# Kernel tuning notes

Measured on AMD Instinct MI355X. Metric: run time of the kernel, lower is better.

## Reference

```python
import jax, jax.numpy as jnp
import numpy as np

TEMPERATURE = 0.07
TIME_THRESH = 5.0 * 1e6  # microseconds


def setup_inputs() -> dict:
    key = jax.random.key(0)
    k1, k2, k3 = jax.random.split(key, 3)
    B, D = 8192, 512
    desc = jax.random.normal(k1, (B, D), dtype=jnp.float32)
    desc = desc / jnp.linalg.norm(desc, axis=-1, keepdims=True)  # module expects normalized descriptors
    seq_ids = jax.random.randint(k2, (B,), 0, 64, dtype=jnp.int64)
    time_mid = jax.random.randint(k3, (B,), 0, 20_000_000, dtype=jnp.int64)
    return {"descriptors": desc, "seq_ids": seq_ids, "time_mid": time_mid}


def reference(descriptors, seq_ids, time_mid):
    B = descriptors.shape[0]
    # [B, B] temperature-scaled cosine similarities
    logits = jnp.matmul(descriptors, descriptors.T) / TEMPERATURE

    eye = jnp.eye(B, dtype=bool)
    same_seq = seq_ids[:, None] == seq_ids[None, :]
    close_time = jnp.abs(time_mid[:, None] - time_mid[None, :]).astype(jnp.float32) < TIME_THRESH
    pos_mask = same_seq & close_time & ~eye  # positives
    offdiag = ~eye                            # positives + negatives = denominator support

    # denominator per row i: log sum_{j != i} exp(logits[i, j])
    denom_lse = jax.nn.logsumexp(jnp.where(offdiag, logits, -jnp.inf), axis=1)  # [B]

    # per positive pair (i, j): -log( exp(l_ij) / denom_i ) = denom_lse_i - l_ij
    pair_loss = jnp.where(pos_mask, denom_lse[:, None] - logits, 0.0)
    num_pos = jnp.sum(pos_mask)
    loss = jnp.sum(pair_loss) / jnp.maximum(num_pos, 1).astype(pair_loss.dtype)
    return loss
```

## Files before the change

kernel.cpp:

```cpp
#include <hip/hip_runtime.h>
#include <math.h>

#define TILE 128

typedef __attribute__((ext_vector_type(4))) float f32x4;
typedef __attribute__((ext_vector_type(2))) long long llong2;

#define INV_T    14.285714285714286f
#define K2C      20.60992915f
#define K2C8     0.32203014296875f
#define INV_T64  0.22321428571428573f
#define TIME_THR 5000000

__device__ __forceinline__ unsigned pack_bf16x2(float lo, float hi) {
  unsigned a = __float_as_uint(lo);
  unsigned b = __float_as_uint(hi);
  a = (a + 0x7FFFu + ((a >> 16) & 1u)) >> 16;
  b = (b + 0x7FFFu + ((b >> 16) & 1u)) & 0xFFFF0000u;
  return b | a;
}

__device__ __forceinline__ unsigned f32_to_e4m3(float x) {
  unsigned u = __float_as_uint(x);
  unsigned s = (u >> 24) & 0x80u;
  int e = (int)((u >> 23) & 0xffu) - 127;
  unsigned m = u & 0x7fffffu;
  if (e < -9) return s;
  if (e < -6) {
    int sh = 20 + (-6 - e);
    unsigned full = (1u << 23) | m;
    unsigned q = full >> sh;
    unsigned rem = full & ((1u << sh) - 1u);
    unsigned half = 1u << (sh - 1);
    if (rem > half || (rem == half && (q & 1u))) q++;
    return s | q;
  }
  unsigned q = m >> 20;
  unsigned rem = m & 0xfffffu;
  if (rem > 0x80000u || (rem == 0x80000u && (q & 1u))) q++;
  int ee = e;
  if (q == 8u) { q = 0u; ee++; }
  if (ee > 8 || (ee == 8 && q == 7u)) return s | 0x7eu;
  return s | (unsigned)((ee + 7) << 3) | q;
}

__device__ __forceinline__ void gl_lds16(const void* g, void* l) {
  __builtin_amdgcn_global_load_lds(
      (const __attribute__((address_space(1))) unsigned int*)g,
      (__attribute__((address_space(3))) unsigned int*)l, 16, 0, 0);
}

template <int MODE>
__device__ __forceinline__ void infonce_body(
    const float* __restrict__ desc, const unsigned char* __restrict__ desc8,
    const int* __restrict__ seq, const int* __restrict__ tmid,
    float* __restrict__ p_se, float* __restrict__ p_ps,
    float* __restrict__ p_pc, int B, int D, int NB) {
  __shared__ __align__(16) unsigned char lA8[2][TILE][64];
  __shared__ __align__(16) unsigned char lB8[2][TILE][64];
  __shared__ int mseq_r[TILE], mtim_r[TILE], mseq_c[TILE], mtim_c[TILE];

  const int T = NB * (NB + 1) / 2;
  int t = blockIdx.x;
  if ((T & 7) == 0) t = (t & 7) * (T >> 3) + (t >> 3);
  float fn = (float)NB + 0.5f;
  int r = (int)(fn - sqrtf(fmaxf(fn * fn - 2.0f * (float)t, 0.0f)));
  if (r < 0) r = 0;
  if (r > NB - 1) r = NB - 1;
  auto Sf = [NB](int rr) { return rr * NB - ((rr * (rr - 1)) >> 1); };
  while (r > 0 && Sf(r) > t) --r;
  while (r < NB - 1 && Sf(r + 1) <= t) ++r;
  const int rb = r;
  const int cb = rb + (t - Sf(rb));
  const bool upper = (cb != rb);

  const int row0 = rb * TILE;
  const int col0 = cb * TILE;

  const int tid = threadIdx.x;
  const int l = tid & 63;
  const int w = tid >> 6;
  const int wrow = (w >> 1) << 6;
  const int wcol = (w & 1) << 6;
  const int lr = l & 15;
  const int kg = l >> 4;

  if (tid < TILE) {
    mseq_r[tid] = seq[row0 + tid];
    mtim_r[tid] = tmid[row0 + tid];
    mseq_c[tid] = seq[col0 + tid];
    mtim_c[tid] = tmid[col0 + tid];
  }

  f32x4 acc[4][4];
#pragma unroll
  for (int m = 0; m < 4; ++m)
#pragma unroll
    for (int n = 0; n < 4; ++n) acc[m][n] = (f32x4){0.f, 0.f, 0.f, 0.f};

  const int NT = D >> 6;

  const int sr = tid >> 3;
  const int sc = tid & 7;

  if (MODE == 2) {
    const unsigned char* pa =
        desc8 + (size_t)(row0 + (tid >> 2)) * D + (tid & 3) * 16;
    const unsigned char* pb =
        desc8 + (size_t)(col0 + (tid >> 2)) * D + (tid & 3) * 16;
    const size_t rstep = (size_t)64 * D;

    auto stageA = [&](int bu_) {
      gl_lds16(pa, (char*)&lA8[bu_][0][0] + tid * 16);
      gl_lds16(pa + rstep, (char*)&lA8[bu_][0][0] + 4096 + tid * 16);
    };
    auto stageB = [&](int bu_) {
      gl_lds16(pb, (char*)&lB8[bu_][0][0] + tid * 16);
      gl_lds16(pb + rstep, (char*)&lB8[bu_][0][0] + 4096 + tid * 16);
    };

    __builtin_amdgcn_sched_barrier(0);
    stageA(0);
    stageB(0);
    __builtin_amdgcn_sched_barrier(0);
    pa += 64;
    pb += 64;

    for (int ts = 0; ts < NT; ++ts) {
      const int bu = ts & 1;
      if (ts + 1 < NT) {
        stageA(bu ^ 1);
        __builtin_amdgcn_sched_barrier(0);
        asm volatile("s_waitcnt vmcnt(2)" ::: "memory");
      } else {
        asm volatile("s_waitcnt vmcnt(0)" ::: "memory");
      }
      __builtin_amdgcn_sched_barrier(0);
      __builtin_amdgcn_s_barrier();
      __builtin_amdgcn_sched_barrier(0);

      llong2 av[4], bv[4];
#pragma unroll
      for (int m = 0; m < 4; ++m) {
        const int row = wrow + (m << 4) + lr;
        const int ch = kg ^ (row & 3);
        av[m] = *reinterpret_cast<const llong2*>(&lA8[bu][row][ch << 4]);
      }
#pragma unroll
      for (int n = 0; n < 4; ++n) {
        const int row = wcol + (n << 4) + lr;
        const int ch = kg ^ (row & 3);
        bv[n] = *reinterpret_cast<const llong2*>(&lB8[bu][row][ch << 4]);
      }
      __builtin_amdgcn_sched_barrier(0);
      if (ts + 1 < NT) stageB(bu ^ 1);
      __builtin_amdgcn_sched_barrier(0);
      pa += 64;
      pb += 64;
      __builtin_amdgcn_sched_barrier(0);
      asm volatile("s_waitcnt lgkmcnt(0)" ::: "memory");
      __builtin_amdgcn_sched_barrier(0);
      __builtin_amdgcn_s_setprio(1);
#pragma unroll
      for (int kk = 0; kk < 2; ++kk)
#pragma unroll
        for (int m = 0; m < 4; ++m)
#pragma unroll
          for (int n = 0; n < 4; ++n)
            acc[m][n] = __builtin_amdgcn_mfma_f32_16x16x32_fp8_fp8(
                av[m][kk], bv[n][kk], acc[m][n], 0, 0, 0);
      __builtin_amdgcn_s_setprio(0);
      __builtin_amdgcn_sched_barrier(0);
      __builtin_amdgcn_s_barrier();
    }
    __syncthreads();
  } else {
    __shared__ __align__(16) unsigned short lAw[TILE][64];
    __shared__ __align__(16) unsigned short lBw[TILE][64];
    typedef __attribute__((ext_vector_type(8))) short short8v;
    for (int k0 = 0; k0 < D; k0 += 64) {
      __syncthreads();
#pragma unroll
      for (int p = 0; p < 4; ++p) {
        const int rr = (p << 5) + sr;
        const float* gA = desc + (size_t)(row0 + rr) * D + k0 + (sc << 3);
        const float4 fa0 = *reinterpret_cast<const float4*>(gA);
        const float4 fa1 = *reinterpret_cast<const float4*>(gA + 4);
        const float* gB = desc + (size_t)(col0 + rr) * D + k0 + (sc << 3);
        const float4 fb0 = *reinterpret_cast<const float4*>(gB);
        const float4 fb1 = *reinterpret_cast<const float4*>(gB + 4);
        uint4 wa, wb;
        wa.x = pack_bf16x2(fa0.x, fa0.y);
        wa.y = pack_bf16x2(fa0.z, fa0.w);
        wa.z = pack_bf16x2(fa1.x, fa1.y);
        wa.w = pack_bf16x2(fa1.z, fa1.w);
        wb.x = pack_bf16x2(fb0.x, fb0.y);
        wb.y = pack_bf16x2(fb0.z, fb0.w);
        wb.z = pack_bf16x2(fb1.x, fb1.y);
        wb.w = pack_bf16x2(fb1.z, fb1.w);
        const int dst = (sc ^ (rr & 7)) << 3;
        *reinterpret_cast<uint4*>(&lAw[rr][dst]) = wa;
        *reinterpret_cast<uint4*>(&lBw[rr][dst]) = wb;
      }
      __syncthreads();
#pragma unroll
      for (int kk = 0; kk < 2; ++kk) {
        short8v af[4], bf[4];
#pragma unroll
        for (int m = 0; m < 4; ++m) {
          const int rowa = wrow + (m << 4) + lr;
          const int ch = ((kk << 2) + kg) ^ (rowa & 7);
          af[m] = *reinterpret_cast<const short8v*>(&lAw[rowa][ch << 3]);
        }
#pragma unroll
        for (int n = 0; n < 4; ++n) {
          const int rowb = wcol + (n << 4) + lr;
          const int ch = ((kk << 2) + kg) ^ (rowb & 7);
          bf[n] = *reinterpret_cast<const short8v*>(&lBw[rowb][ch << 3]);
        }
#pragma unroll
        for (int m = 0; m < 4; ++m)
#pragma unroll
          for (int n = 0; n < 4; ++n)
            acc[m][n] = __builtin_amdgcn_mfma_f32_16x16x32_bf16(af[m], bf[n],
                                                                acc[m][n], 0, 0, 0);
      }
    }
    __syncthreads();
  }

  float* rowred = (float*)&lA8[0][0][0];
  float* colred = (float*)&lB8[0][0][0];

  const float kmul = (MODE == 2) ? K2C8 : K2C;
  const float psc = (MODE == 2) ? INV_T64 : INV_T;

  int cseq[4], ctim[4], gcol[4];
#pragma unroll
  for (int n = 0; n < 4; ++n) {
    const int cl = wcol + (n << 4) + lr;
    cseq[n] = mseq_c[cl];
    ctim[n] = mtim_c[cl];
    gcol[n] = col0 + cl;
  }
  float colse[4] = {0.f, 0.f, 0.f, 0.f};
  float colpd[4] = {0.f, 0.f, 0.f, 0.f};
  float colpc[4] = {0.f, 0.f, 0.f, 0.f};

#pragma unroll
  for (int m = 0; m < 4; ++m) {
#pragma unroll
    for (int reg = 0; reg < 4; ++reg) {
      const int rl = wrow + (m << 4) + (kg << 2) + reg;
      const int growg = row0 + rl;
      const int rs = mseq_r[rl];
      const int rt = mtim_r[rl];
      float se = 0.f, pd = 0.f, pcnt = 0.f;
#pragma unroll
      for (int n = 0; n < 4; ++n) {
        const float dot = acc[m][n][reg];
        const float e = exp2f(fmaf(dot, kmul, -K2C));
        const bool nd = (growg != gcol[n]);
        int dt = rt - ctim[n];
        dt = dt < 0 ? -dt : dt;
        const bool pos = nd && (rs == cseq[n]) && (dt < TIME_THR);
        const float ev = nd ? e : 0.f;
        const float dv = pos ? dot : 0.f;
        const float cv = pos ? 1.f : 0.f;
        se += ev;
        pd += dv;
        pcnt += cv;
        if (upper) {
          colse[n] += ev;
          colpd[n] += dv;
          colpc[n] += cv;
        }
      }
#pragma unroll
      for (int s = 1; s < 16; s <<= 1) {
        se += __shfl_xor(se, s);
        pd += __shfl_xor(pd, s);
        pcnt += __shfl_xor(pcnt, s);
      }
      if ((l & 15) == 0) {
        if (MODE == 2) {
          const int half = wcol >> 6;
          float* rr3 = rowred + ((size_t)(half * TILE + rl)) * 3;
          rr3[0] = se;
          rr3[1] = pd;
          rr3[2] = pcnt;
        } else {
          atomicAdd(&p_se[growg], se);
          atomicAdd(&p_ps[growg], pd * psc);
          atomicAdd(&p_pc[growg], pcnt);
        }
      }
    }
  }
  if (upper) {
#pragma unroll
    for (int n = 0; n < 4; ++n) {
      float cs = colse[n], cp = colpd[n], cc = colpc[n];
      cs += __shfl_xor(cs, 16);
      cp += __shfl_xor(cp, 16);
      cc += __shfl_xor(cc, 16);
      cs += __shfl_xor(cs, 32);
      cp += __shfl_xor(cp, 32);
      cc += __shfl_xor(cc, 32);
      if (kg == 0) {
        if (MODE == 2) {
          const int half = wrow >> 6;
          const int cl = wcol + (n << 4) + lr;
          float* cr3 = colred + ((size_t)(half * TILE + cl)) * 3;
          cr3[0] = cs;
          cr3[1] = cp;
          cr3[2] = cc;
        } else {
          atomicAdd(&p_se[gcol[n]], cs);
          atomicAdd(&p_ps[gcol[n]], cp * psc);
          atomicAdd(&p_pc[gcol[n]], cc);
        }
      }
    }
  }

  if (MODE == 2) {
    __syncthreads();
    if (tid < TILE) {
      const int row = tid;
      const float se = rowred[(size_t)row * 3 + 0] + rowred[(size_t)(TILE + row) * 3 + 0];
      const float pd = rowred[(size_t)row * 3 + 1] + rowred[(size_t)(TILE + row) * 3 + 1];
      const float pc = rowred[(size_t)row * 3 + 2] + rowred[(size_t)(TILE + row) * 3 + 2];
      const size_t o = (size_t)cb * B + row0 + row;
      p_se[o] = se;
      p_ps[o] = pd * INV_T64;
      p_pc[o] = pc;
    } else if (upper && tid < 2 * TILE) {
      const int col = tid - TILE;
      const float se = colred[(size_t)col * 3 + 0] + colred[(size_t)(TILE + col) * 3 + 0];
      const float pd = colred[(size_t)col * 3 + 1] + colred[(size_t)(TILE + col) * 3 + 1];
      const float pc = colred[(size_t)col * 3 + 2] + colred[(size_t)(TILE + col) * 3 + 2];
      const size_t o = (size_t)rb * B + col0 + col;
      p_se[o] = se;
      p_ps[o] = pd * INV_T64;
      p_pc[o] = pc;
    }
  }
}

__global__ __launch_bounds__(256, 2) void infonce_main2(
    const float* desc, const unsigned char* desc8, const int* seq,
    const int* tmid, float* p_se, float* p_ps, float* p_pc, int B, int D,
    int NB) {
  infonce_body<2>(desc, desc8, seq, tmid, p_se, p_ps, p_pc, B, D, NB);
}
__global__ __launch_bounds__(256, 2) void infonce_main0(
    const float* desc, const unsigned char* desc8, const int* seq,
    const int* tmid, float* p_se, float* p_ps, float* p_pc, int B, int D,
    int NB) {
  infonce_body<0>(desc, desc8, seq, tmid, p_se, p_ps, p_pc, B, D, NB);
}

__global__ __launch_bounds__(256) void conv_fp8(const float* __restrict__ in,
                                                unsigned char* __restrict__ out,
                                                int D, int nchunk) {
  const int u = blockIdx.x * 256 + threadIdx.x;
  if (u >= nchunk) return;
  const int cpr = D >> 4;
  const int r = u / cpr;
  const int cc = u - r * cpr;
  const int kb = cc >> 2;
  const int c = cc & 3;
  const int kg = c ^ (r & 3);
  const float* src = in + (size_t)r * D + kb * 64 + kg * 8;
  const float4 f0 = *reinterpret_cast<const float4*>(src);
  const float4 f1 = *reinterpret_cast<const float4*>(src + 4);
  const float4 g0 = *reinterpret_cast<const float4*>(src + 32);
  const float4 g1 = *reinterpret_cast<const float4*>(src + 36);
  unsigned char b[16];
  b[0] = f32_to_e4m3(f0.x * 8.f);
  b[1] = f32_to_e4m3(f0.y * 8.f);
  b[2] = f32_to_e4m3(f0.z * 8.f);
  b[3] = f32_to_e4m3(f0.w * 8.f);
  b[4] = f32_to_e4m3(f1.x * 8.f);
  b[5] = f32_to_e4m3(f1.y * 8.f);
  b[6] = f32_to_e4m3(f1.z * 8.f);
  b[7] = f32_to_e4m3(f1.w * 8.f);
  b[8] = f32_to_e4m3(g0.x * 8.f);
  b[9] = f32_to_e4m3(g0.y * 8.f);
  b[10] = f32_to_e4m3(g0.z * 8.f);
  b[11] = f32_to_e4m3(g0.w * 8.f);
  b[12] = f32_to_e4m3(g1.x * 8.f);
  b[13] = f32_to_e4m3(g1.y * 8.f);
  b[14] = f32_to_e4m3(g1.z * 8.f);
  b[15] = f32_to_e4m3(g1.w * 8.f);
  uint4 wv;
  unsigned* wp = (unsigned*)&wv;
#pragma unroll
  for (int d = 0; d < 4; ++d)
    wp[d] = (unsigned)b[d * 4] | ((unsigned)b[d * 4 + 1] << 8) |
            ((unsigned)b[d * 4 + 2] << 16) | ((unsigned)b[d * 4 + 3] << 24);
  *reinterpret_cast<uint4*>(out + (size_t)u * 16) = wv;
}

__global__ __launch_bounds__(256) void reduce_parts4(
    const float* __restrict__ p_se, const float* __restrict__ p_ps,
    const float* __restrict__ p_pc, float* __restrict__ bnum,
    float* __restrict__ bcnt, int B, int NB) {
  const int tid = threadIdx.x;
  const int rloc = tid & 63;
  const int chunk = tid >> 6;
  const int row = blockIdx.x * 64 + rloc;
  const int jpc = NB >> 2;
  float se = 0.f, ps = 0.f, pc = 0.f;
  for (int j = chunk * jpc; j < (chunk + 1) * jpc; ++j) {
    const size_t o = (size_t)j * B + row;
    se += p_se[o];
    ps += p_ps[o];
    pc += p_pc[o];
  }
  __shared__ float s3[3][4][64];
  s3[0][chunk][rloc] = se;
  s3[1][chunk][rloc] = ps;
  s3[2][chunk][rloc] = pc;
  __syncthreads();
  if (tid < 64) {
    const float tse = s3[0][0][tid] + s3[0][1][tid] + s3[0][2][tid] + s3[0][3][tid];
    const float tps = s3[1][0][tid] + s3[1][1][tid] + s3[1][2][tid] + s3[1][3][tid];
    const float tpc = s3[2][0][tid] + s3[2][1][tid] + s3[2][2][tid] + s3[2][3][tid];
    float a = tpc * (logf(tse) + INV_T) - tps;
    float b = tpc;
#pragma unroll
    for (int s = 1; s < 64; s <<= 1) {
      a += __shfl_xor(a, s);
      b += __shfl_xor(b, s);
    }
    if (tid == 0) {
      bnum[blockIdx.x] = a;
      bcnt[blockIdx.x] = b;
    }
  }
}

__global__ __launch_bounds__(256) void final_reduce(
    const float* __restrict__ bnum, const float* __restrict__ bcnt,
    float* __restrict__ out, int n) {
  __shared__ float sn[256];
  __shared__ float sc[256];
  const int tid = threadIdx.x;
  float a = 0.f, b = 0.f;
  for (int i = tid; i < n; i += 256) {
    a += bnum[i];
    b += bcnt[i];
  }
  sn[tid] = a;
  sc[tid] = b;
  __syncthreads();
  for (int s = 128; s > 0; s >>= 1) {
    if (tid < s) {
      sn[tid] += sn[tid + s];
      sc[tid] += sc[tid + s];
    }
    __syncthreads();
  }
  if (tid == 0) out[0] = sn[0] / fmaxf(sc[0], 1.f);
}

__global__ __launch_bounds__(1024) void infonce_finalize(
    const float* __restrict__ a_se, const float* __restrict__ a_ps,
    const float* __restrict__ a_pc, float* __restrict__ out, int B) {
  __shared__ float sn[1024];
  __shared__ float sc[1024];
  const int tid = threadIdx.x;
  float num = 0.f, cnt = 0.f;
  for (int i = tid; i < B; i += 1024) {
    const float c = a_pc[i];
    num += c * (logf(a_se[i]) + INV_T) - a_ps[i];
    cnt += c;
  }
  sn[tid] = num;
  sc[tid] = cnt;
  __syncthreads();
  for (int s = 512; s > 0; s >>= 1) {
    if (tid < s) {
      sn[tid] += sn[tid + s];
      sc[tid] += sc[tid + s];
    }
    __syncthreads();
  }
  if (tid == 0) out[0] = sn[0] / fmaxf(sc[0], 1.f);
}

extern "C" void kernel_launch(void* const* d_in, const int* in_sizes, int n_in,
                              void* d_out, int out_size, void* d_ws, size_t ws_size,
                              hipStream_t stream) {
  (void)n_in;
  (void)out_size;
  const float* desc = (const float*)d_in[0];
  const int* seq = (const int*)d_in[1];
  const int* tmid = (const int*)d_in[2];
  const int B = in_sizes[1];
  const int D = in_sizes[0] / B;
  const int NB = B / TILE;
  const int T = NB * (NB + 1) / 2;

  const size_t desc8_bytes = (size_t)B * D;
  const size_t parts_elems = (size_t)B * NB;
  const size_t nb1 = (size_t)B / 64;
  const size_t need8 = desc8_bytes + 3 * parts_elems * 4 + 2 * nb1 * 4;

  if ((B & 255) == 0 && (D & 63) == 0 && ws_size >= need8) {
    unsigned char* desc8 = (unsigned char*)d_ws;
    float* p_se = (float*)((char*)d_ws + desc8_bytes);
    float* p_ps = p_se + parts_elems;
    float* p_pc = p_ps + parts_elems;
    float* bnum = p_pc + parts_elems;
    float* bcnt = bnum + nb1;
    const int nchunk = (int)(((size_t)B * D) >> 4);
    conv_fp8<<<(nchunk + 255) / 256, 256, 0, stream>>>(desc, desc8, D, nchunk);
    infonce_main2<<<T, 256, 0, stream>>>(desc, desc8, seq, tmid, p_se, p_ps,
                                         p_pc, B, D, NB);
    if ((NB & 3) == 0 && (B & 63) == 0) {
      const int nrb = B / 64;
      reduce_parts4<<<nrb, 256, 0, stream>>>(p_se, p_ps, p_pc, bnum, bcnt, B, NB);
      final_reduce<<<1, 256, 0, stream>>>(bnum, bcnt, (float*)d_out, nrb);
    } else {
      const int nrb = B / 64;
      reduce_parts4<<<nrb, 256, 0, stream>>>(p_se, p_ps, p_pc, bnum, bcnt, B, NB);
      final_reduce<<<1, 256, 0, stream>>>(bnum, bcnt, (float*)d_out, nrb);
    }
  } else {
    float* a_se = (float*)d_ws;
    float* a_ps = a_se + B;
    float* a_pc = a_ps + B;
    hipMemsetAsync(d_ws, 0, (size_t)3 * B * sizeof(float), stream);
    infonce_main0<<<T, 256, 0, stream>>>(desc, nullptr, seq, tmid, a_se, a_ps,
                                         a_pc, B, D, NB);
    infonce_finalize<<<1, 1024, 0, stream>>>(a_se, a_ps, a_pc, (float*)d_out, B);
  }
}
```

Baseline: 95.66 us.

## Triple-buffer fp8 LDS staging and change swizzle to reduce bank conflicts

```diff
diff --git a/kernel.cpp b/kernel.cpp
--- a/kernel.cpp
+++ b/kernel.cpp
@@ -56,8 +56,8 @@
     const int* __restrict__ seq, const int* __restrict__ tmid,
     float* __restrict__ p_se, float* __restrict__ p_ps,
     float* __restrict__ p_pc, int B, int D, int NB) {
-  __shared__ __align__(16) unsigned char lA8[2][TILE][64];
-  __shared__ __align__(16) unsigned char lB8[2][TILE][64];
+  __shared__ __align__(16) unsigned char lA8[3][TILE][64];
+  __shared__ __align__(16) unsigned char lB8[3][TILE][64];
   __shared__ int mseq_r[TILE], mtim_r[TILE], mseq_c[TILE], mtim_c[TILE];
 
   const int T = NB * (NB + 1) / 2;
@@ -110,28 +110,29 @@
         desc8 + (size_t)(col0 + (tid >> 2)) * D + (tid & 3) * 16;
     const size_t rstep = (size_t)64 * D;
 
-    auto stageA = [&](int bu_) {
-      gl_lds16(pa, (char*)&lA8[bu_][0][0] + tid * 16);
-      gl_lds16(pa + rstep, (char*)&lA8[bu_][0][0] + 4096 + tid * 16);
+    auto stage = [&](int bu_, int tt) {
+      const int off = tt << 6;
+      gl_lds16(pa + off, (char*)&lA8[bu_][0][0] + tid * 16);
+      gl_lds16(pa + off + rstep, (char*)&lA8[bu_][0][0] + 4096 + tid * 16);
+      gl_lds16(pb + off, (char*)&lB8[bu_][0][0] + tid * 16);
+      gl_lds16(pb + off + rstep, (char*)&lB8[bu_][0][0] + 4096 + tid * 16);
     };
-    auto stageB = [&](int bu_) {
-      gl_lds16(pb, (char*)&lB8[bu_][0][0] + tid * 16);
-      gl_lds16(pb + rstep, (char*)&lB8[bu_][0][0] + 4096 + tid * 16);
-    };
 
     __builtin_amdgcn_sched_barrier(0);
-    stageA(0);
-    stageB(0);
+    stage(0, 0);
+    if (NT > 1) stage(1, 1);
     __builtin_amdgcn_sched_barrier(0);
-    pa += 64;
-    pb += 64;
-
+
+    int bu = 0;
     for (int ts = 0; ts < NT; ++ts) {
-      const int bu = ts & 1;
-      if (ts + 1 < NT) {
-        stageA(bu ^ 1);
+      if (ts + 2 < NT) {
+        int sbu = bu + 2;
+        if (sbu >= 3) sbu -= 3;
+        stage(sbu, ts + 2);
         __builtin_amdgcn_sched_barrier(0);
-        asm volatile("s_waitcnt vmcnt(2)" ::: "memory");
+        asm volatile("s_waitcnt vmcnt(8)" ::: "memory");
+      } else if (ts + 1 < NT) {
+        asm volatile("s_waitcnt vmcnt(4)" ::: "memory");
       } else {
         asm volatile("s_waitcnt vmcnt(0)" ::: "memory");
       }
@@ -143,20 +144,15 @@
 #pragma unroll
       for (int m = 0; m < 4; ++m) {
         const int row = wrow + (m << 4) + lr;
-        const int ch = kg ^ (row & 3);
+        const int ch = kg ^ ((row + (row >> 2)) & 3);
         av[m] = *reinterpret_cast<const llong2*>(&lA8[bu][row][ch << 4]);
       }
 #pragma unroll
       for (int n = 0; n < 4; ++n) {
         const int row = wcol + (n << 4) + lr;
-        const int ch = kg ^ (row & 3);
+        const int ch = kg ^ ((row + (row >> 2)) & 3);
         bv[n] = *reinterpret_cast<const llong2*>(&lB8[bu][row][ch << 4]);
       }
-      __builtin_amdgcn_sched_barrier(0);
-      if (ts + 1 < NT) stageB(bu ^ 1);
-      __builtin_amdgcn_sched_barrier(0);
-      pa += 64;
-      pb += 64;
       __builtin_amdgcn_sched_barrier(0);
       asm volatile("s_waitcnt lgkmcnt(0)" ::: "memory");
       __builtin_amdgcn_sched_barrier(0);
@@ -172,6 +168,7 @@
       __builtin_amdgcn_s_setprio(0);
       __builtin_amdgcn_sched_barrier(0);
       __builtin_amdgcn_s_barrier();
+      bu = bu == 2 ? 0 : bu + 1;
     }
     __syncthreads();
   } else {
@@ -371,7 +368,7 @@
   const int cc = u - r * cpr;
   const int kb = cc >> 2;
   const int c = cc & 3;
-  const int kg = c ^ (r & 3);
+  const int kg = c ^ ((r + (r >> 2)) & 3);
   const float* src = in + (size_t)r * D + kb * 64 + kg * 8;
   const float4 f0 = *reinterpret_cast<const float4*>(src);
   const float4 f1 = *reinterpret_cast<const float4*>(src + 4);
@@ -520,15 +517,9 @@
     conv_fp8<<<(nchunk + 255) / 256, 256, 0, stream>>>(desc, desc8, D, nchunk);
     infonce_main2<<<T, 256, 0, stream>>>(desc, desc8, seq, tmid, p_se, p_ps,
                                          p_pc, B, D, NB);
-    if ((NB & 3) == 0 && (B & 63) == 0) {
-      const int nrb = B / 64;
-      reduce_parts4<<<nrb, 256, 0, stream>>>(p_se, p_ps, p_pc, bnum, bcnt, B, NB);
-      final_reduce<<<1, 256, 0, stream>>>(bnum, bcnt, (float*)d_out, nrb);
-    } else {
-      const int nrb = B / 64;
-      reduce_parts4<<<nrb, 256, 0, stream>>>(p_se, p_ps, p_pc, bnum, bcnt, B, NB);
-      final_reduce<<<1, 256, 0, stream>>>(bnum, bcnt, (float*)d_out, nrb);
-    }
+    const int nrb = B / 64;
+    reduce_parts4<<<nrb, 256, 0, stream>>>(p_se, p_ps, p_pc, bnum, bcnt, B, NB);
+    final_reduce<<<1, 256, 0, stream>>>(bnum, bcnt, (float*)d_out, nrb);
   } else {
     float* a_se = (float*)d_ws;
     float* a_ps = a_se + B;
```

After: 98.74 us. 3.2% more time.
